# Optimization experiments

Measured on AMD Instinct MI355X. Metric: run time of the kernel, lower is better.

Reference implementation:

```python
import jax, jax.numpy as jnp
import numpy as np
from jax import lax

B, T_Y, T_X = 16, 1600, 400
MEL_C, TXT_C, MAS_C = 80, 512, 384
HID = MAS_C * 2          # SwiGLUConvFFN hidden width (mas_channels*2)
NEG = -1e9


def setup_inputs() -> dict:
    key = jax.random.key(0)
    ks = jax.random.split(key, 20)
    p = lambda k, s: jax.random.normal(k, s, jnp.float32) * 0.02
    return {
        "mel_hidden_states": jax.random.normal(ks[0], (B, T_Y, MEL_C), jnp.float32),
        "text_hidden_states": jax.random.normal(ks[1], (B, T_X, TXT_C), jnp.float32),
        # mel SwiGLU conv-FFN (kernel 5): in->2*HID, gate, HID->MAS_C
        "mel_w1": p(ks[2], (2 * HID, MEL_C, 5)), "mel_b1": jnp.zeros((2 * HID,), jnp.float32),
        "mel_w2": p(ks[3], (MAS_C, HID, 5)),     "mel_b2": jnp.zeros((MAS_C,), jnp.float32),
        # text SwiGLU conv-FFN (kernel 3)
        "txt_w1": p(ks[4], (2 * HID, TXT_C, 3)), "txt_b1": jnp.zeros((2 * HID,), jnp.float32),
        "txt_w2": p(ks[5], (MAS_C, HID, 3)),     "txt_b2": jnp.zeros((MAS_C,), jnp.float32),
        # SimpleAttention query/key projections (value proj does not affect returned outputs)
        "wq": p(ks[6], (MAS_C, MAS_C)), "bq": jnp.zeros((MAS_C,), jnp.float32),
        "wk": p(ks[7], (MAS_C, MAS_C)), "bk": jnp.zeros((MAS_C,), jnp.float32),
        "x_lens": jax.random.randint(ks[8], (B,), T_X // 2, T_X + 1).astype(jnp.int32),
        "y_lens": jax.random.randint(ks[9], (B,), T_Y // 2, T_Y + 1).astype(jnp.int32),
    }


def _conv_ffn(x, pad_mask, w1, b1, w2, b2):
    """SwiGLU/ReGLU conv FFN. x:(B,T,C), pad_mask:(B,T) True=padded."""
    keep = (~pad_mask)[:, None, :].astype(x.dtype)          # (B,1,T)
    h = jnp.transpose(x, (0, 2, 1)) * keep                  # (B,C,T)
    dn = ("NCH", "OIH", "NCH")
    h = lax.conv_general_dilated(h, w1, (1,), "SAME", dimension_numbers=dn) + b1[None, :, None]
    a, g = jnp.split(h, 2, axis=1)
    h = a * jax.nn.relu(g) * keep                           # relugt gating
    h = lax.conv_general_dilated(h, w2, (1,), "SAME", dimension_numbers=dn) + b2[None, :, None]
    return jnp.transpose(h * keep, (0, 2, 1))               # (B,T,out)


def _mas_single(logp, t_x, t_y):
    """Glow-TTS maximum_path for one item. logp:(T_X,T_Y). Returns hard path (T_X,T_Y)."""
    xi = jnp.arange(T_X)
    yi = jnp.arange(T_Y)
    valid = (xi[:, None] < t_x) & (yi[None, :] < t_y) & (xi[:, None] <= yi[None, :])
    lp = jnp.where(valid, logp, NEG)

    def fstep(prev, col):                                   # prev:(T_X,), col:(T_X,)
        shifted = jnp.concatenate([jnp.full((1,), NEG, prev.dtype), prev[:-1]])
        cur = col + jnp.maximum(prev, shifted)
        return cur, cur

    init = jnp.where(xi == 0, 0.0, NEG).astype(logp.dtype)
    _, v = lax.scan(fstep, init, lp.T)                      # v:(T_Y,T_X) DP table

    def bstep(x, y):                                        # backtrack from y=T_Y-1 down
        active = y < t_y
        row = (xi == x) & active
        vp = v[y - 1]
        dec = (x > 0) & ((x == y) | (vp[jnp.maximum(x - 1, 0)] > vp[x]))
        new_x = jnp.where(active & (y > 0) & dec, x - 1, x)
        return new_x, row

    _, rows = lax.scan(bstep, t_x - 1, jnp.arange(T_Y - 1, -1, -1))
    return rows[::-1].T.astype(jnp.float32)                 # (T_X,T_Y)


def _safe_log(t, eps=1e-6):
    return jnp.nan_to_num(jnp.log(t + eps), nan=eps)


def reference(mel_hidden_states, text_hidden_states,
              mel_w1, mel_b1, mel_w2, mel_b2,
              txt_w1, txt_b1, txt_w2, txt_b2,
              wq, bq, wk, bk, x_lens, y_lens):
    x_mask = jnp.arange(T_X)[None, :] >= x_lens[:, None]    # (B,T_X) True=padded
    y_mask = jnp.arange(T_Y)[None, :] >= y_lens[:, None]    # (B,T_Y)

    text_proj = _conv_ffn(text_hidden_states, x_mask, txt_w1, txt_b1, txt_w2, txt_b2)
    mel_proj = _conv_ffn(mel_hidden_states, y_mask, mel_w1, mel_b1, mel_w2, mel_b2)

    q = mel_proj @ wq.T + bq                                # (B,T_Y,D)
    k = text_proj @ wk.T + bk                               # (B,T_X,D)
    scores = jnp.einsum("byd,bxd->byx", q, k) / (MAS_C ** 0.5)
    # expand_masks: mask==0 only where query AND key are both padded (faithful to source)
    both_pad = y_mask[:, :, None] & x_mask[:, None, :]
    scores = jnp.where(both_pad, jnp.float32(-1e-9), scores)
    attn_w = jax.nn.softmax(scores, axis=-1)                # (B,T_Y,T_X)

    avg_attn = attn_w[:, None]                              # (B,1,T_Y,T_X)
    attn_logprob = _safe_log(avg_attn)

    mas_in = jnp.transpose(attn_logprob[:, 0], (0, 2, 1))   # (B,T_X,T_Y)
    attn_hard = lax.stop_gradient(jax.vmap(_mas_single)(mas_in, x_lens, y_lens))
    attn_hard_dur = attn_hard.sum(2)                        # (B,T_X)
    return avg_attn, attn_logprob, attn_hard, attn_hard_dur
```

## Files before the change

kernel.cpp:

```cpp
#include <hip/hip_runtime.h>
#include <cstdint>

#define B 16
#define TY 1600
#define TX 400
#define MAS 384
#define HID 768
#define NEGV -1e9f

typedef __bf16 bf16x8 __attribute__((ext_vector_type(8)));
typedef float  f32x4  __attribute__((ext_vector_type(4)));
typedef float  f32x16 __attribute__((ext_vector_type(16)));

__device__ __forceinline__ f32x4 mfma16(bf16x8 a, bf16x8 b, f32x4 c) {
  return __builtin_amdgcn_mfma_f32_16x16x32_bf16(a, b, c, 0, 0, 0);
}
__device__ __forceinline__ f32x16 mfma32(bf16x8 a, bf16x8 b, f32x16 c) {
  return __builtin_amdgcn_mfma_f32_32x32x16_bf16(a, b, c, 0, 0, 0);
}

__global__ void split_pad_k(const float* __restrict__ in, __bf16* __restrict__ oh,
                            __bf16* __restrict__ ol, int CIN, int CINP, long n) {
  long i = (long)blockIdx.x * 256 + threadIdx.x;
  if (i >= n) return;
  long row = i / CINP; int ci = (int)(i - row * CINP);
  float v = (ci < CIN) ? in[row * CIN + ci] : 0.f;
  __bf16 h = (__bf16)v;
  oh[i] = h; ol[i] = (__bf16)(v - (float)h);
}

__global__ void wsplit_k(const float* __restrict__ w, __bf16* __restrict__ oh,
                         __bf16* __restrict__ ol, int CIN, int K_, int CINP, long n) {
  long i = (long)blockIdx.x * 256 + threadIdx.x;
  if (i >= n) return;
  long kdspan = (long)K_ * CINP;
  long nn = i / kdspan; int kd = (int)(i - nn * kdspan);
  int k = kd / CINP, ci = kd - k * CINP;
  float v = (ci < CIN) ? w[(nn * CIN + ci) * K_ + k] : 0.f;
  __bf16 h = (__bf16)v;
  oh[i] = h; ol[i] = (__bf16)(v - (float)h);
}

__global__ void tsplit_k(const float* __restrict__ in, __bf16* __restrict__ oh,
                         __bf16* __restrict__ ol, int JTOT, long n) {
  long i = (long)blockIdx.x * 256 + threadIdx.x;
  if (i >= n) return;
  int m = (int)(i / JTOT), j = (int)(i - (long)m * JTOT);
  float v = in[i];
  long o = (long)j * 384 + m;
  __bf16 h = (__bf16)v;
  oh[o] = h; ol[o] = (__bf16)(v - (float)h);
}

__global__ void fold_bias_k(const float* __restrict__ wq, const float* __restrict__ b,
                            float* __restrict__ o) {
  int n = threadIdx.x;
  float s = 0.f;
  for (int m = 0; m < 384; ++m) s = fmaf(wq[n * 384 + m], b[m], s);
  o[n] = s;
}

template<int KK>
__global__ __launch_bounds__(256)
void fold_mfma(const __bf16* __restrict__ xh, const __bf16* __restrict__ xl,
               const __bf16* __restrict__ wh, const __bf16* __restrict__ wl,
               __bf16* __restrict__ oh, __bf16* __restrict__ ol)
{
  constexpr int CINP = 384, ROWS = 64, STRIDE = 65;
  __shared__ float4 xs[8 * STRIDE];
  const int t0 = blockIdx.x * 64, n0 = blockIdx.y * 128;
  const int tid = threadIdx.x, wn = tid >> 6, lane = tid & 63;
  const int lr = lane & 15, lg = lane >> 4;
  const f32x4 Z4 = {0.f, 0.f, 0.f, 0.f};
  f32x4 acc[4][2];
  #pragma unroll
  for (int m = 0; m < 4; ++m) { acc[m][0] = Z4; acc[m][1] = Z4; }

  #pragma unroll 1
  for (int ci0 = 0; ci0 < CINP; ci0 += 32) {
    __syncthreads();
    for (int e = tid; e < ROWS * 8; e += 256) {
      int row = e >> 3, sc = e & 7, spl = sc >> 2, cg = sc & 3;
      int t = t0 + row;
      xs[(spl * 4 + cg) * STRIDE + row] =
          *(const float4*)((spl ? xl : xh) + (size_t)t * CINP + ci0 + cg * 8);
    }
    __syncthreads();
    bf16x8 ah[4], al[4];
    #pragma unroll
    for (int mf = 0; mf < 4; ++mf) {
      int row = mf * 16 + lr;
      ah[mf] = *(const bf16x8*)&xs[lg * STRIDE + row];
      al[mf] = *(const bf16x8*)&xs[(4 + lg) * STRIDE + row];
    }
    size_t kd = (size_t)ci0 + lg * 8;
    bf16x8 bh[2], bl[2];
    #pragma unroll
    for (int nf = 0; nf < 2; ++nf) {
      int nc = n0 + wn * 32 + nf * 16 + lr;
      bh[nf] = *(const bf16x8*)(wh + (size_t)nc * 384 + kd);
      bl[nf] = *(const bf16x8*)(wl + (size_t)nc * 384 + kd);
    }
    #pragma unroll
    for (int nf = 0; nf < 2; ++nf)
      #pragma unroll
      for (int mf = 0; mf < 4; ++mf) acc[mf][nf] = mfma16(ah[mf], bh[nf], acc[mf][nf]);
    #pragma unroll
    for (int nf = 0; nf < 2; ++nf)
      #pragma unroll
      for (int mf = 0; mf < 4; ++mf) acc[mf][nf] = mfma16(ah[mf], bl[nf], acc[mf][nf]);
    #pragma unroll
    for (int nf = 0; nf < 2; ++nf)
      #pragma unroll
      for (int mf = 0; mf < 4; ++mf) acc[mf][nf] = mfma16(al[mf], bh[nf], acc[mf][nf]);
  }
  #pragma unroll
  for (int nf = 0; nf < 2; ++nf) {
    int c = n0 + wn * 32 + nf * 16 + lr;
    #pragma unroll
    for (int mf = 0; mf < 4; ++mf) {
      #pragma unroll
      for (int r = 0; r < 4; ++r) {
        int j = t0 + mf * 16 + lg * 4 + r;
        int k = j % KK, ci = j / KK;
        size_t o = (size_t)((((ci >> 4) * KK + k) * 2 + ((ci >> 3) & 1)) * 3072)
                 + (size_t)c * 8 + (ci & 7);
        float v = acc[mf][nf][r];
        __bf16 vh = (__bf16)v;
        oh[o] = vh; ol[o] = (__bf16)(v - (float)vh);
      }
    }
  }
}

template<int CINP, int K, int T>
__global__ __launch_bounds__(256)
void conv1_mfma(const __bf16* __restrict__ xh, const __bf16* __restrict__ xl,
                const __bf16* __restrict__ wh, const __bf16* __restrict__ wl,
                const float* __restrict__ bias, const int* __restrict__ lens,
                __bf16* __restrict__ hh, __bf16* __restrict__ hl)
{
  constexpr int BM = 128, PAD = K / 2, ROWS = BM + K - 1, KD = K * CINP;
  __shared__ float4 xs[8 * ROWS];
  const int b = blockIdx.z, t0 = blockIdx.x * BM, n0 = blockIdx.y * 64;
  const int tid = threadIdx.x, wid = tid >> 6, lane = tid & 63;
  const int wm = wid >> 1, wn = wid & 1, lr = lane & 15, lg = lane >> 4;
  const int len = lens[b];
  const f32x4 Z4 = {0.f, 0.f, 0.f, 0.f};
  f32x4 acc_a[4][2], acc_g[4][2];
  #pragma unroll
  for (int m = 0; m < 4; ++m)
    #pragma unroll
    for (int n = 0; n < 2; ++n) { acc_a[m][n] = Z4; acc_g[m][n] = Z4; }

  #pragma unroll 1
  for (int ci0 = 0; ci0 < CINP; ci0 += 32) {
    __syncthreads();
    for (int e = tid; e < ROWS * 8; e += 256) {
      int row = e >> 3, sc = e & 7, spl = sc >> 2, cg = sc & 3;
      int t = t0 + row - PAD;
      float4 v = {0.f, 0.f, 0.f, 0.f};
      if (t >= 0 && t < len)
        v = *(const float4*)((spl ? xl : xh) + ((size_t)b * T + t) * CINP + ci0 + cg * 8);
      xs[(spl * 4 + cg) * ROWS + row] = v;
    }
    __syncthreads();
    #pragma unroll
    for (int k = 0; k < K; ++k) {
      bf16x8 ah[4], al[4];
      #pragma unroll
      for (int mf = 0; mf < 4; ++mf) {
        int row = wm * 64 + mf * 16 + lr + k;
        ah[mf] = *(const bf16x8*)&xs[lg * ROWS + row];
        al[mf] = *(const bf16x8*)&xs[(4 + lg) * ROWS + row];
      }
      size_t kd = (size_t)k * CINP + ci0 + lg * 8;
      #pragma unroll
      for (int nf = 0; nf < 2; ++nf) {
        int na = n0 + wn * 32 + nf * 16 + lr;
        bf16x8 bah = *(const bf16x8*)(wh + (size_t)na * KD + kd);
        bf16x8 bal = *(const bf16x8*)(wl + (size_t)na * KD + kd);
        bf16x8 bgh = *(const bf16x8*)(wh + (size_t)(na + HID) * KD + kd);
        bf16x8 bgl = *(const bf16x8*)(wl + (size_t)(na + HID) * KD + kd);
        #pragma unroll
        for (int mf = 0; mf < 4; ++mf) {
          acc_a[mf][nf] = mfma16(ah[mf], bah, acc_a[mf][nf]);
          acc_a[mf][nf] = mfma16(ah[mf], bal, acc_a[mf][nf]);
          acc_a[mf][nf] = mfma16(al[mf], bah, acc_a[mf][nf]);
          acc_g[mf][nf] = mfma16(ah[mf], bgh, acc_g[mf][nf]);
          acc_g[mf][nf] = mfma16(ah[mf], bgl, acc_g[mf][nf]);
          acc_g[mf][nf] = mfma16(al[mf], bgh, acc_g[mf][nf]);
        }
      }
    }
  }
  #pragma unroll
  for (int nf = 0; nf < 2; ++nf) {
    int c = n0 + wn * 32 + nf * 16 + lr;
    float ba = bias[c], bg = bias[c + HID];
    #pragma unroll
    for (int mf = 0; mf < 4; ++mf) {
      #pragma unroll
      for (int r = 0; r < 4; ++r) {
        int t = t0 + wm * 64 + mf * 16 + lg * 4 + r;
        if (t < T) {
          float a = acc_a[mf][nf][r] + ba;
          float g = acc_g[mf][nf][r] + bg;
          float v = a * fmaxf(g, 0.f);
          __bf16 vh = (__bf16)v;
          size_t o = ((size_t)b * T + t) * HID + c;
          hh[o] = vh;
          hl[o] = (__bf16)(v - (float)vh);
        }
      }
    }
  }
}

template<int K, int T, bool STORET>
__global__ __launch_bounds__(256)
void conv2_mfma(const __bf16* __restrict__ xh, const __bf16* __restrict__ xl,
                const __bf16* __restrict__ wh, const __bf16* __restrict__ wl,
                const float* __restrict__ bias, const float* __restrict__ ab,
                const int* __restrict__ lens, float* __restrict__ out)
{
  constexpr int CINP = 768, BM = 128, PAD = K / 2, ROWS = BM + K - 1, STRIDE = ROWS + 1;
  constexpr int BROWS = K * 2;
  __shared__ float4 xa[4 * STRIDE];
  __shared__ float4 bs[2 * BROWS * 192];
  const int b = blockIdx.z, t0 = blockIdx.x * BM, n0 = blockIdx.y * 192;
  const int tid = threadIdx.x, wid = tid >> 6, lane = tid & 63;
  const int wm = wid >> 1, wn = wid & 1, lc = lane & 31, lk = lane >> 5;
  const int len = lens[b];
  f32x16 acc[2][3];
  #pragma unroll
  for (int m = 0; m < 2; ++m)
    #pragma unroll
    for (int n = 0; n < 3; ++n)
      #pragma unroll
      for (int r = 0; r < 16; ++r) acc[m][n][r] = 0.f;

  #pragma unroll 1
  for (int s = 0; s < 48; ++s) {
    __syncthreads();
    for (int e = tid; e < ROWS * 4; e += 256) {
      int row = e >> 2, sc = e & 3, spl = sc >> 1, cg = sc & 1;
      int t = t0 + row - PAD;
      float4 v = {0.f, 0.f, 0.f, 0.f};
      if (t >= 0 && t < len)
        v = *(const float4*)((spl ? xl : xh) + ((size_t)b * T + t) * CINP + s * 16 + cg * 8);
      xa[(spl * 2 + cg) * STRIDE + row] = v;
    }
    for (int r = wid; r < 2 * BROWS; r += 4) {
      int spl = r / BROWS, rr = r - spl * BROWS;
      const char* src = (const char*)((spl ? wl : wh) + (size_t)(s * BROWS + rr) * 3072
                                      + (size_t)n0 * 8) + (size_t)lane * 16;
      char* dst = (char*)&bs[r * 192];
      #pragma unroll
      for (int i = 0; i < 3; ++i)
        __builtin_amdgcn_global_load_lds(
            (const __attribute__((address_space(1))) void*)(src + i * 1024),
            (__attribute__((address_space(3))) void*)(dst + i * 1024), 16, 0, 0);
    }
    __syncthreads();
    #pragma unroll
    for (int k = 0; k < K; ++k) {
      bf16x8 ah[2], al[2], bh[3], bl[3];
      #pragma unroll
      for (int mf = 0; mf < 2; ++mf) {
        int row = wm * 64 + mf * 32 + lc + k;
        ah[mf] = *(const bf16x8*)&xa[lk * STRIDE + row];
        al[mf] = *(const bf16x8*)&xa[(2 + lk) * STRIDE + row];
      }
      #pragma unroll
      for (int nf = 0; nf < 3; ++nf) {
        int col = wn * 96 + nf * 32 + lc;
        bh[nf] = *(const bf16x8*)&bs[(k * 2 + lk) * 192 + col];
        bl[nf] = *(const bf16x8*)&bs[(BROWS + k * 2 + lk) * 192 + col];
      }
      #pragma unroll
      for (int nf = 0; nf < 3; ++nf)
        #pragma unroll
        for (int mf = 0; mf < 2; ++mf)
          acc[mf][nf] = mfma32(ah[mf], bh[nf], acc[mf][nf]);
      #pragma unroll
      for (int nf = 0; nf < 3; ++nf)
        #pragma unroll
        for (int mf = 0; mf < 2; ++mf)
          acc[mf][nf] = mfma32(ah[mf], bl[nf], acc[mf][nf]);
      #pragma unroll
      for (int nf = 0; nf < 3; ++nf)
        #pragma unroll
        for (int mf = 0; mf < 2; ++mf)
          acc[mf][nf] = mfma32(al[mf], bh[nf], acc[mf][nf]);
    }
  }
  #pragma unroll
  for (int nf = 0; nf < 3; ++nf) {
    int c = n0 + wn * 96 + nf * 32 + lc;
    float bb = bias[c], aB = ab[c];
    #pragma unroll
    for (int mf = 0; mf < 2; ++mf) {
      #pragma unroll
      for (int r = 0; r < 16; ++r) {
        int t = t0 + wm * 64 + mf * 32 + (r & 3) + 8 * (r >> 2) + 4 * lk;
        if (t < T) {
          float v = acc[mf][nf][r] + bb;
          if (t >= len) v = 0.f;
          v += aB;
          if (STORET) out[((size_t)b * MAS + c) * T + t] = v;
          else        out[((size_t)b * T + t) * MAS + c] = v;
        }
      }
    }
  }
}

__global__ __launch_bounds__(512)
void scores_k(const float* __restrict__ q, const float* __restrict__ kT,
              const int* __restrict__ xl, const int* __restrict__ yl,
              float* __restrict__ oattn, float* __restrict__ ologp)
{
  __shared__ float qs[16 * 384];
  __shared__ float tmp[8];
  const int b = blockIdx.y, y0 = blockIdx.x * 16, tid = threadIdx.x;
  for (int e = tid; e < 16 * 384; e += 512)
    qs[e] = q[((size_t)b * TY + (y0 + e / 384)) * 384 + (e - (e / 384) * 384)];
  __syncthreads();
  float acc[16];
  #pragma unroll
  for (int i = 0; i < 16; ++i) acc[i] = 0.f;
  const int x = tid;
  if (x < TX) {
    const float* kb = kT + (size_t)b * MAS * TX + x;
    for (int d = 0; d < 384; d += 4) {
      float k0 = kb[(size_t)(d + 0) * TX], k1 = kb[(size_t)(d + 1) * TX];
      float k2 = kb[(size_t)(d + 2) * TX], k3 = kb[(size_t)(d + 3) * TX];
      #pragma unroll
      for (int yy = 0; yy < 16; ++yy) {
        float4 qv = *(const float4*)&qs[yy * 384 + d];
        acc[yy] = fmaf(qv.x, k0, fmaf(qv.y, k1, fmaf(qv.z, k2, fmaf(qv.w, k3, acc[yy]))));
      }
    }
  }
  const int xlen = xl[b], ylen = yl[b];
  const float scale = 0.05103103630798288f;
  const bool xpad = (x >= xlen);
  const int wv = tid >> 6, ln = tid & 63;
  #pragma unroll 1
  for (int yy = 0; yy < 16; ++yy) {
    int y = y0 + yy;
    float s = -3.0e38f;
    if (x < TX) {
      s = acc[yy] * scale;
      if (xpad && (y >= ylen)) s = -1e-9f;
    }
    float m = s;
    for (int off = 32; off; off >>= 1) m = fmaxf(m, __shfl_xor(m, off));
    if (ln == 0) tmp[wv] = m;
    __syncthreads();
    float mx = fmaxf(fmaxf(fmaxf(tmp[0], tmp[1]), fmaxf(tmp[2], tmp[3])),
                     fmaxf(fmaxf(tmp[4], tmp[5]), fmaxf(tmp[6], tmp[7])));
    __syncthreads();
    float e = (x < TX) ? expf(s - mx) : 0.f;
    float sm = e;
    for (int off = 32; off; off >>= 1) sm += __shfl_xor(sm, off);
    if (ln == 0) tmp[wv] = sm;
    __syncthreads();
    float tot = tmp[0] + tmp[1] + tmp[2] + tmp[3] + tmp[4] + tmp[5] + tmp[6] + tmp[7];
    __syncthreads();
    if (x < TX) {
      float w = e / tot;
      size_t o = ((size_t)b * TY + y) * TX + x;
      oattn[o] = w;
      ologp[o] = logf(w + 1e-6f);
    }
  }
}

__global__ __launch_bounds__(64, 1)
void mas_k(const float* __restrict__ logprob, const int* __restrict__ xl,
           const int* __restrict__ yl, float* __restrict__ hard, float* __restrict__ dur)
{
  __shared__ float ring[12800];
  __shared__ unsigned char lbits[102400];
  const int b = blockIdx.x;
  const int lane = threadIdx.x;
  const int xlen = xl[b], ylen = yl[b];
  const float* lpb = logprob + (size_t)b * TY * TX;
  const int p0 = lane * 8 - 4;
  int t;
  t = p0;     if (t < 0) t = 0; if (t > 396) t = 396; const int lb0 = t;
  t = p0 + 4; if (t < 0) t = 0; if (t > 396) t = 396; const int lb1 = t;
  t = p0 + 8; if (t < 0) t = 0; if (t > 396) t = 396; const int lb2 = t;

  float w[12], wxm[12];
  #pragma unroll
  for (int i = 0; i < 12; ++i) {
    int p = p0 + i;
    wxm[i] = (p >= 0 && p < xlen) ? 0.f : NEGV;
    w[i] = (p == 0) ? 0.f : NEGV;
  }

  const char* lpc = (const char*)lpb;
  constexpr size_t maxgs = (size_t)TY * 1600 - 25600;
  char* ringc = (char*)ring;
  auto issue_group = [&](int g) {
    size_t gs = (size_t)g * 25600; if (gs > maxgs) gs = maxgs;
    const char* src = lpc + gs + (size_t)lane * 16;
    char* dst = ringc + (g & 1) * 25600;
    #pragma unroll
    for (int i = 0; i < 25; ++i)
      __builtin_amdgcn_global_load_lds(
          (const __attribute__((address_space(1))) void*)(src + i * 1024),
          (__attribute__((address_space(3))) void*)(dst + i * 1024), 16, 0, 0);
  };

  issue_group(0);
  issue_group(1);

  const int ngroups = (ylen + 15) >> 4;
  #pragma unroll 1
  for (int g = 0; g < ngroups; ++g) {
    asm volatile("s_waitcnt vmcnt(25)" ::: "memory");
    __builtin_amdgcn_sched_barrier(0);
    const float* half = ring + (g & 1) * 6400;
    const int ybase = g * 16;
    const bool phase1 = (ybase < TX);
    unsigned long long bitsacc = 0ULL;
    #pragma unroll
    for (int d = 0; d < 4; ++d) {
      float h0 = __shfl_up(w[8], 1),  h1 = __shfl_up(w[9], 1);
      float h2 = __shfl_up(w[10], 1), h3 = __shfl_up(w[11], 1);
      w[0] = lane ? h0 : NEGV; w[1] = lane ? h1 : NEGV;
      w[2] = lane ? h2 : NEGV; w[3] = lane ? h3 : NEGV;
      #pragma unroll
      for (int r = 0; r < 4; ++r) {
        const int row = d * 4 + r;
        const int y = ybase + row;
        const float4 v0 = *(const float4*)&half[row * 400 + lb0];
        const float4 v1 = *(const float4*)&half[row * 400 + lb1];
        const float4 v2 = *(const float4*)&half[row * 400 + lb2];
        float lp[12] = {v0.x + wxm[0], v0.y + wxm[1], v0.z + wxm[2],  v0.w + wxm[3],
                        v1.x + wxm[4], v1.y + wxm[5], v1.z + wxm[6],  v1.w + wxm[7],
                        v2.x + wxm[8], v2.y + wxm[9], v2.z + wxm[10], v2.w + wxm[11]};
        if (phase1) {
          int c = y - p0;
          #pragma unroll
          for (int i = 0; i < 12; ++i) lp[i] = (i <= c) ? lp[i] : NEGV;
        }
        unsigned byte = 0;
        #pragma unroll
        for (int j = 0; j < 8; ++j)
          byte |= (w[j + 3] > w[j + 4]) ? (1u << j) : 0u;
        bitsacc |= (unsigned long long)byte << (((d & 1) * 4 + r) * 8);
        float nw[12];
        nw[0] = lp[0] + w[0];
        #pragma unroll
        for (int i = 1; i < 12; ++i) nw[i] = lp[i] + fmaxf(w[i], w[i - 1]);
        #pragma unroll
        for (int i = 0; i < 12; ++i) w[i] = nw[i];
      }
      if (d & 1) {
        *(unsigned long long*)&lbits[(size_t)((ybase >> 3) + (d >> 1)) * 512 + (size_t)lane * 8] = bitsacc;
        bitsacc = 0ULL;
      }
    }
    __builtin_amdgcn_sched_barrier(0);
    issue_group(g + 2);
  }

  __syncthreads();

  int x = xlen - 1;
  int cnt = 0;
  float* hb = hard + (size_t)b * TX * TY;
  float* db = dur + (size_t)b * TX;

  #pragma unroll 1
  for (int ycur = ylen - 1; ycur >= 0; ycur -= 64) {
    int lo = x - 63; if (lo < 0) lo = 0;
    const int wb = (lo >> 3) & ~3;
    int ry = ycur - lane;
    unsigned w0 = 0, w1 = 0, w2 = 0;
    if (ry >= 0) {
      const unsigned char* p = lbits + (size_t)(ry >> 3) * 512 + (ry & 7);
      unsigned bt_[12];
      #pragma unroll
      for (int j = 0; j < 12; ++j) bt_[j] = p[(size_t)(wb + j) * 8];
      w0 = bt_[0] | (bt_[1] << 8) | (bt_[2] << 16) | (bt_[3] << 24);
      w1 = bt_[4] | (bt_[5] << 8) | (bt_[6] << 16) | (bt_[7] << 24);
      w2 = bt_[8] | (bt_[9] << 8) | (bt_[10] << 16) | (bt_[11] << 24);
    }
    const int rows = (ycur + 1 < 64) ? (ycur + 1) : 64;
    #pragma unroll 1
    for (int s = 0; s < rows; s += 8) {
      const int cnt8 = (rows - s < 8) ? (rows - s) : 8;
      unsigned r0[8], r1[8], r2[8];
      #pragma unroll
      for (int u = 0; u < 8; ++u) {
        r0[u] = (unsigned)__builtin_amdgcn_readlane((int)w0, s + u);
        r1[u] = (unsigned)__builtin_amdgcn_readlane((int)w1, s + u);
        r2[u] = (unsigned)__builtin_amdgcn_readlane((int)w2, s + u);
      }
      #pragma unroll
      for (int u = 0; u < 8; ++u) {
        if (u < cnt8) {
          const int yy = ycur - s - u;
          ++cnt;
          if (yy > 0 && x > 0) {
            const int boff = (x >> 3) - wb;
            const unsigned word = (boff < 4) ? r0[u] : ((boff < 8) ? r1[u] : r2[u]);
            const unsigned byte = word >> ((boff & 3) * 8);
            if ((x == yy) || ((byte >> (x & 7)) & 1)) {
              for (int q = lane; q < cnt; q += 64) hb[(size_t)x * TY + yy + q] = 1.0f;
              if (lane == 0) db[x] = (float)cnt;
              cnt = 0;
              --x;
            }
          }
        }
      }
    }
  }
  for (int q = lane; q < cnt; q += 64) hb[(size_t)x * TY + q] = 1.0f;
  if (lane == 0) db[x] = (float)cnt;
}

extern "C" void kernel_launch(void* const* d_in, const int* in_sizes, int n_in,
                              void* d_out, int out_size, void* d_ws, size_t ws_size,
                              hipStream_t stream) {
  const float* mel_x  = (const float*)d_in[0];
  const float* txt_x  = (const float*)d_in[1];
  const float* mel_w1 = (const float*)d_in[2];
  const float* mel_b1 = (const float*)d_in[3];
  const float* mel_w2 = (const float*)d_in[4];
  const float* mel_b2 = (const float*)d_in[5];
  const float* txt_w1 = (const float*)d_in[6];
  const float* txt_b1 = (const float*)d_in[7];
  const float* txt_w2 = (const float*)d_in[8];
  const float* txt_b2 = (const float*)d_in[9];
  const float* wq     = (const float*)d_in[10];
  const float* bq     = (const float*)d_in[11];
  const float* wk     = (const float*)d_in[12];
  const float* bk     = (const float*)d_in[13];
  const int*   xl     = (const int*)d_in[14];
  const int*   yl     = (const int*)d_in[15];

  char* wsb = (char*)d_ws;
  constexpr size_t MXH   = 0;
  constexpr size_t MXL   = MXH   + 4915200;
  constexpr size_t TXH   = MXL   + 4915200;
  constexpr size_t TXL   = TXH   + 6553600;
  constexpr size_t KTF   = TXH;
  constexpr size_t WFMH  = TXL   + 6553600;
  constexpr size_t WFML  = WFMH  + 2949120;
  constexpr size_t WFTH  = WFML  + 2949120;
  constexpr size_t WFTL  = WFTH  + 1769472;
  constexpr size_t B2M   = WFTL  + 1769472;
  constexpr size_t B2T   = B2M   + 2048;
  constexpr size_t HH    = B2T   + 2048;
  constexpr size_t HL    = HH    + 39321600;
  constexpr size_t SCR   = HL    + 39321600;
  constexpr size_t W1MH  = SCR;
  constexpr size_t W1ML  = W1MH  + 1474560;
  constexpr size_t W1TH  = W1ML  + 1474560;
  constexpr size_t W1TL  = W1TH  + 4718592;
  constexpr size_t WQH   = W1TL  + 4718592;
  constexpr size_t WQL   = WQH   + 294912;
  constexpr size_t WKH   = WQL   + 294912;
  constexpr size_t WKL   = WKH   + 294912;
  constexpr size_t W2TMH = WKL   + 294912;
  constexpr size_t W2TML = W2TMH + 2949120;
  constexpr size_t W2TTH = W2TML + 2949120;
  constexpr size_t W2TTL = W2TTH + 1769472;
  constexpr size_t QF    = SCR;

  float* out = (float*)d_out;
  float* o_attn = out;
  float* o_logp = out + (size_t)10240000;
  float* o_hard = out + (size_t)20480000;
  float* o_dur  = out + (size_t)30720000;

  hipMemsetAsync(o_hard, 0, (size_t)(10240000 + 6400) * sizeof(float), stream);

  split_pad_k<<<9600, 256, 0, stream>>>(mel_x, (__bf16*)(wsb + MXH), (__bf16*)(wsb + MXL), 80, 96, 2457600L);
  split_pad_k<<<12800, 256, 0, stream>>>(txt_x, (__bf16*)(wsb + TXH), (__bf16*)(wsb + TXL), 512, 512, 3276800L);
  wsplit_k<<<2880, 256, 0, stream>>>(mel_w1, (__bf16*)(wsb + W1MH), (__bf16*)(wsb + W1ML), 80, 5, 96, 737280L);
  wsplit_k<<<9216, 256, 0, stream>>>(txt_w1, (__bf16*)(wsb + W1TH), (__bf16*)(wsb + W1TL), 512, 3, 512, 2359296L);
  wsplit_k<<<576, 256, 0, stream>>>(wq, (__bf16*)(wsb + WQH), (__bf16*)(wsb + WQL), 384, 1, 384, 147456L);
  wsplit_k<<<576, 256, 0, stream>>>(wk, (__bf16*)(wsb + WKH), (__bf16*)(wsb + WKL), 384, 1, 384, 147456L);
  tsplit_k<<<5760, 256, 0, stream>>>(mel_w2, (__bf16*)(wsb + W2TMH), (__bf16*)(wsb + W2TML), 3840, 1474560L);
  tsplit_k<<<3456, 256, 0, stream>>>(txt_w2, (__bf16*)(wsb + W2TTH), (__bf16*)(wsb + W2TTL), 2304, 884736L);
  fold_mfma<5><<<dim3(60, 3), 256, 0, stream>>>(
      (const __bf16*)(wsb + W2TMH), (const __bf16*)(wsb + W2TML),
      (const __bf16*)(wsb + WQH), (const __bf16*)(wsb + WQL),
      (__bf16*)(wsb + WFMH), (__bf16*)(wsb + WFML));
  fold_mfma<3><<<dim3(36, 3), 256, 0, stream>>>(
      (const __bf16*)(wsb + W2TTH), (const __bf16*)(wsb + W2TTL),
      (const __bf16*)(wsb + WKH), (const __bf16*)(wsb + WKL),
      (__bf16*)(wsb + WFTH), (__bf16*)(wsb + WFTL));
  fold_bias_k<<<1, 384, 0, stream>>>(wq, mel_b2, (float*)(wsb + B2M));
  fold_bias_k<<<1, 384, 0, stream>>>(wk, txt_b2, (float*)(wsb + B2T));

  conv1_mfma<512, 3, 400><<<dim3(4, 12, B), 256, 0, stream>>>(
      (const __bf16*)(wsb + TXH), (const __bf16*)(wsb + TXL),
      (const __bf16*)(wsb + W1TH), (const __bf16*)(wsb + W1TL),
      txt_b1, xl, (__bf16*)(wsb + HH), (__bf16*)(wsb + HL));
  conv2_mfma<3, 400, true><<<dim3(4, 2, B), 256, 0, stream>>>(
      (const __bf16*)(wsb + HH), (const __bf16*)(wsb + HL),
      (const __bf16*)(wsb + WFTH), (const __bf16*)(wsb + WFTL),
      (const float*)(wsb + B2T), bk, xl, (float*)(wsb + KTF));

  conv1_mfma<96, 5, 1600><<<dim3(13, 12, B), 256, 0, stream>>>(
      (const __bf16*)(wsb + MXH), (const __bf16*)(wsb + MXL),
      (const __bf16*)(wsb + W1MH), (const __bf16*)(wsb + W1ML),
      mel_b1, yl, (__bf16*)(wsb + HH), (__bf16*)(wsb + HL));
  conv2_mfma<5, 1600, false><<<dim3(13, 2, B), 256, 0, stream>>>(
      (const __bf16*)(wsb + HH), (const __bf16*)(wsb + HL),
      (const __bf16*)(wsb + WFMH), (const __bf16*)(wsb + WFML),
      (const float*)(wsb + B2M), bq, yl, (float*)(wsb + QF));

  scores_k<<<dim3(100, B), 512, 0, stream>>>(
      (const float*)(wsb + QF), (const float*)(wsb + KTF), xl, yl, o_attn, o_logp);
  mas_k<<<B, 64, 0, stream>>>(o_logp, xl, yl, o_hard, o_dur);
}
```

Before: 1.528 ms.

## Spread MAS forward DP over four waves with LDS halo exchange

The MAS forward dynamic programme moves from a single 64-lane wave, where each lane owned 8 text positions, to a 256-thread block where each thread owns 2 positions. Neighbour values crossing wave boundaries now go through a double-buffered LDS halo with a block barrier every 4 rows instead of a shuffle, and the backpointer bits are packed with cross-lane shuffles. The global-to-LDS prefetch is split across the four waves with per-wave waitcnt values. This shortens each thread's serial work per row, but it adds a __syncthreads per 4 rows, and with only 16 blocks the kernel stays latency bound.

Result: faster. 1.455 ms (-4.8%).

```diff
diff --git a/kernel.cpp b/kernel.cpp
--- a/kernel.cpp
+++ b/kernel.cpp
@@ -378,99 +378,118 @@
   }
 }
 
-__global__ __launch_bounds__(64, 1)
+__global__ __launch_bounds__(256, 1)
 void mas_k(const float* __restrict__ logprob, const int* __restrict__ xl,
            const int* __restrict__ yl, float* __restrict__ hard, float* __restrict__ dur)
 {
   __shared__ float ring[12800];
   __shared__ unsigned char lbits[102400];
+  __shared__ float vbuf[2][400];
   const int b = blockIdx.x;
-  const int lane = threadIdx.x;
+  const int tid = threadIdx.x, wid = tid >> 6;
+  const int GL = tid;
   const int xlen = xl[b], ylen = yl[b];
   const float* lpb = logprob + (size_t)b * TY * TX;
-  const int p0 = lane * 8 - 4;
-  int t;
-  t = p0;     if (t < 0) t = 0; if (t > 396) t = 396; const int lb0 = t;
-  t = p0 + 4; if (t < 0) t = 0; if (t > 396) t = 396; const int lb1 = t;
-  t = p0 + 8; if (t < 0) t = 0; if (t > 396) t = 396; const int lb2 = t;
-
-  float w[12], wxm[12];
-  #pragma unroll
-  for (int i = 0; i < 12; ++i) {
-    int p = p0 + i;
-    wxm[i] = (p >= 0 && p < xlen) ? 0.f : NEGV;
-    w[i] = (p == 0) ? 0.f : NEGV;
+  const int p0 = GL * 2 - 4;
+
+  int a0 = p0, a1 = p0 + 2, a2 = p0 + 4;
+  a0 = a0 < 0 ? 0 : (a0 > 398 ? 398 : a0);
+  a1 = a1 < 0 ? 0 : (a1 > 398 ? 398 : a1);
+  a2 = a2 < 0 ? 0 : (a2 > 398 ? 398 : a2);
+
+  float w[6], wxm[6];
+  #pragma unroll
+  for (int j = 0; j < 6; ++j) {
+    int x = p0 + j;
+    wxm[j] = (x >= 0 && x < xlen) ? 0.f : NEGV;
+    w[j] = (x == 0) ? 0.f : NEGV;
   }
 
   const char* lpc = (const char*)lpb;
   constexpr size_t maxgs = (size_t)TY * 1600 - 25600;
   char* ringc = (char*)ring;
+  const int lane = tid & 63;
   auto issue_group = [&](int g) {
     size_t gs = (size_t)g * 25600; if (gs > maxgs) gs = maxgs;
-    const char* src = lpc + gs + (size_t)lane * 16;
-    char* dst = ringc + (g & 1) * 25600;
-    #pragma unroll
-    for (int i = 0; i < 25; ++i)
+    for (int c = wid; c < 25; c += 4)
       __builtin_amdgcn_global_load_lds(
-          (const __attribute__((address_space(1))) void*)(src + i * 1024),
-          (__attribute__((address_space(3))) void*)(dst + i * 1024), 16, 0, 0);
+          (const __attribute__((address_space(1))) void*)(lpc + gs + (size_t)c * 1024 + (size_t)lane * 16),
+          (__attribute__((address_space(3))) void*)(ringc + (g & 1) * 25600 + c * 1024), 16, 0, 0);
   };
 
   issue_group(0);
   issue_group(1);
 
+  int pb = 0;
+  unsigned p16 = 0;
   const int ngroups = (ylen + 15) >> 4;
   #pragma unroll 1
   for (int g = 0; g < ngroups; ++g) {
-    asm volatile("s_waitcnt vmcnt(25)" ::: "memory");
+    if (wid == 0) asm volatile("s_waitcnt vmcnt(7)" ::: "memory");
+    else          asm volatile("s_waitcnt vmcnt(6)" ::: "memory");
     __builtin_amdgcn_sched_barrier(0);
+    __syncthreads();
     const float* half = ring + (g & 1) * 6400;
     const int ybase = g * 16;
     const bool phase1 = (ybase < TX);
-    unsigned long long bitsacc = 0ULL;
-    #pragma unroll
-    for (int d = 0; d < 4; ++d) {
-      float h0 = __shfl_up(w[8], 1),  h1 = __shfl_up(w[9], 1);
-      float h2 = __shfl_up(w[10], 1), h3 = __shfl_up(w[11], 1);
-      w[0] = lane ? h0 : NEGV; w[1] = lane ? h1 : NEGV;
-      w[2] = lane ? h2 : NEGV; w[3] = lane ? h3 : NEGV;
+    #pragma unroll
+    for (int sb = 0; sb < 4; ++sb) {
       #pragma unroll
       for (int r = 0; r < 4; ++r) {
-        const int row = d * 4 + r;
+        const int row = sb * 4 + r;
         const int y = ybase + row;
-        const float4 v0 = *(const float4*)&half[row * 400 + lb0];
-        const float4 v1 = *(const float4*)&half[row * 400 + lb1];
-        const float4 v2 = *(const float4*)&half[row * 400 + lb2];
-        float lp[12] = {v0.x + wxm[0], v0.y + wxm[1], v0.z + wxm[2],  v0.w + wxm[3],
-                        v1.x + wxm[4], v1.y + wxm[5], v1.z + wxm[6],  v1.w + wxm[7],
-                        v2.x + wxm[8], v2.y + wxm[9], v2.z + wxm[10], v2.w + wxm[11]};
+        const float2 d0 = *(const float2*)&half[row * 400 + a0];
+        const float2 d1 = *(const float2*)&half[row * 400 + a1];
+        const float2 d2 = *(const float2*)&half[row * 400 + a2];
+        float lp[6] = {d0.x + wxm[0], d0.y + wxm[1], d1.x + wxm[2],
+                       d1.y + wxm[3], d2.x + wxm[4], d2.y + wxm[5]};
         if (phase1) {
           int c = y - p0;
           #pragma unroll
-          for (int i = 0; i < 12; ++i) lp[i] = (i <= c) ? lp[i] : NEGV;
+          for (int j = 0; j < 6; ++j) lp[j] = (j <= c) ? lp[j] : NEGV;
         }
-        unsigned byte = 0;
-        #pragma unroll
-        for (int j = 0; j < 8; ++j)
-          byte |= (w[j + 3] > w[j + 4]) ? (1u << j) : 0u;
-        bitsacc |= (unsigned long long)byte << (((d & 1) * 4 + r) * 8);
-        float nw[12];
+        unsigned pr = ((w[3] > w[4]) ? 1u : 0u) | ((w[4] > w[5]) ? 2u : 0u);
+        p16 |= pr << ((y & 7) * 2);
+        float nw[6];
         nw[0] = lp[0] + w[0];
         #pragma unroll
-        for (int i = 1; i < 12; ++i) nw[i] = lp[i] + fmaxf(w[i], w[i - 1]);
+        for (int j = 1; j < 6; ++j) nw[j] = lp[j] + fmaxf(w[j], w[j - 1]);
         #pragma unroll
-        for (int i = 0; i < 12; ++i) w[i] = nw[i];
-      }
-      if (d & 1) {
-        *(unsigned long long*)&lbits[(size_t)((ybase >> 3) + (d >> 1)) * 512 + (size_t)lane * 8] = bitsacc;
-        bitsacc = 0ULL;
-      }
+        for (int j = 0; j < 6; ++j) w[j] = nw[j];
+      }
+      if (sb & 1) {
+        const int y7 = ybase + sb * 4 + 3;
+        unsigned lo = 0, hi = 0;
+        #pragma unroll
+        for (int r2 = 0; r2 < 4; ++r2) {
+          lo |= ((p16 >> (2 * r2)) & 3u) << (8 * r2);
+          hi |= ((p16 >> (2 * r2 + 8)) & 3u) << (8 * r2);
+        }
+        unsigned lo1 = (unsigned)__shfl_xor((int)lo, 1), hi1 = (unsigned)__shfl_xor((int)hi, 1);
+        lo |= lo1 << 2; hi |= hi1 << 2;
+        unsigned lo2 = (unsigned)__shfl_xor((int)lo, 2), hi2 = (unsigned)__shfl_xor((int)hi, 2);
+        lo |= lo2 << 4; hi |= hi2 << 4;
+        if ((GL & 3) == 0 && GL < 200) {
+          unsigned long long E = (unsigned long long)lo | ((unsigned long long)hi << 32);
+          *(unsigned long long*)&lbits[(size_t)(y7 >> 3) * 512 + (size_t)(GL >> 2) * 8] = E;
+        }
+        p16 = 0;
+      }
+      if (GL < 200) { vbuf[pb][2 * GL] = w[4]; vbuf[pb][2 * GL + 1] = w[5]; }
+      __syncthreads();
+      #pragma unroll
+      for (int j = 0; j < 4; ++j) {
+        int x = p0 + j;
+        w[j] = (x >= 0 && GL < 200) ? vbuf[pb][x] : NEGV;
+      }
+      pb ^= 1;
     }
     __builtin_amdgcn_sched_barrier(0);
     issue_group(g + 2);
   }
 
   __syncthreads();
+  if (wid != 0) return;
 
   int x = xlen - 1;
   int cnt = 0;
@@ -623,5 +642,5 @@
 
   scores_k<<<dim3(100, B), 512, 0, stream>>>(
       (const float*)(wsb + QF), (const float*)(wsb + KTF), xl, yl, o_attn, o_logp);
-  mas_k<<<B, 64, 0, stream>>>(o_logp, xl, yl, o_hard, o_dur);
-}
+  mas_k<<<B, 256, 0, stream>>>(o_logp, xl, yl, o_hard, o_dur);
+}
```
